# Kernel tuning notes

Hardware: AMD Instinct MI355X
Metric: run time of the kernel (lower is better)

## Reference

```python
import jax, jax.numpy as jnp
import numpy as np

ETA = 3.0
KCAP = 96
POS_W = 1.2
LAMBDA_CD = 1.0
LAMBDA_P0 = 1.0
STRIDES = (8.0, 16.0, 32.0)


def _level_terms(pred_reg, pred_obj, pred_cls, gt, stride):
    """Vectorized per-level version of the triple python loop.
    pred_reg: [B,6,H,W], pred_obj/pred_cls: [B,1,H,W], gt: [B,Ng,3,2].
    Returns partial sums (reg, obj, cls, pos_count, neg_count)."""
    B, _, H, W = pred_obj.shape
    HW = H * W
    Ng = gt.shape[1]
    ys = (jnp.arange(H, dtype=jnp.float32) + 0.5) * stride
    xs = (jnp.arange(W, dtype=jnp.float32) + 0.5) * stride
    yy, xx = jnp.meshgrid(ys, xs, indexing='ij')
    px = xx.reshape(-1)  # [HW]
    py = yy.reshape(-1)
    P = px[None, None, :]  # [1,1,HW]
    Q = py[None, None, :]
    # triangle vertices, each [B,Ng,1] for broadcasting against HW
    Ax, Ay = gt[:, :, 0, 0:1], gt[:, :, 0, 1:2]
    Bx, By = gt[:, :, 1, 0:1], gt[:, :, 1, 1:2]
    Cx, Cy = gt[:, :, 2, 0:1], gt[:, :, 2, 1:2]

    def sgn(x1, y1, x2, y2, x3, y3):
        return (x1 - x3) * (y2 - y3) - (x2 - x3) * (y1 - y3)

    d1 = sgn(P, Q, Ax, Ay, Bx, By)
    d2 = sgn(P, Q, Bx, By, Cx, Cy)
    d3 = sgn(P, Q, Cx, Cy, Ax, Ay)
    has_neg = (d1 < 0) | (d2 < 0) | (d3 < 0)
    has_pos = (d1 > 0) | (d2 > 0) | (d3 > 0)
    inside = ~(has_neg & has_pos)  # [B,Ng,HW]

    def segd(x1, y1, x2, y2):
        vx, vy = x2 - x1, y2 - y1
        wx, wy = P - x1, Q - y1
        t = jnp.clip((wx * vx + wy * vy) / (vx * vx + vy * vy + 1e-9), 0.0, 1.0)
        dx = P - (x1 + t * vx)
        dy = Q - (y1 + t * vy)
        return jnp.sqrt(dx * dx + dy * dy + 1e-12)

    dist = jnp.minimum(segd(Ax, Ay, Bx, By),
                       jnp.minimum(segd(Bx, By, Cx, Cy), segd(Cx, Cy, Ax, Ay)))
    pos = inside | (dist <= ETA)  # [B,Ng,HW]

    # top-k cap: keep the KCAP positives with smallest boundary distance
    dmask = jnp.where(pos, dist, jnp.inf)
    negd, idx = jax.lax.top_k(-dmask, KCAP)  # [B,Ng,K]
    keep = jnp.isfinite(negd)                # finite <=> was a positive
    bi = jnp.arange(B)[:, None, None]
    gi = jnp.arange(Ng)[None, :, None]
    capped = jnp.zeros((B, Ng, HW), dtype=bool).at[bi, gi, idx].set(keep)
    m = capped.astype(jnp.float32)
    pos_count = m.sum()

    # objectness BCE-with-logits (pos_weight) over the whole map
    obj_t = capped.any(axis=1).astype(jnp.float32)  # [B,HW]
    x = pred_obj.reshape(B, HW)
    obj_loss = (POS_W * obj_t * jax.nn.softplus(-x)
                + (1.0 - obj_t) * jax.nn.softplus(x)).sum()
    neg_count = jnp.float32(B * HW) - obj_t.sum()

    pred_off = pred_reg.transpose(0, 2, 3, 1).reshape(B, HW, 3, 2)
    centers = jnp.stack([px, py], axis=-1)  # [HW,2]
    gt_off = (gt[:, :, None] - centers[None, None, :, None]) / stride  # [B,Ng,HW,3,2]
    p0 = ((pred_off[:, None, :, 0] - gt_off[:, :, :, 0]) ** 2).sum(-1)  # [B,Ng,HW]
    pp = pred_off[:, None, :, 1:, :]  # [B,1,HW,2,2]
    gg = gt_off[:, :, :, 1:, :]       # [B,Ng,HW,2,2]
    d = jnp.sqrt(((pp[..., :, None, :] - gg[..., None, :, :]) ** 2).sum(-1))  # [B,Ng,HW,2,2]
    cd = d.min(-1).sum(-1) + d.min(-2).sum(-1)  # [B,Ng,HW]
    reg = (m * (LAMBDA_P0 * p0 + LAMBDA_CD * cd)).sum()

    # class BCE on positives only, target = 1
    cls = (m * jax.nn.softplus(-pred_cls.reshape(B, 1, HW))).sum()
    return reg, obj_loss, cls, pos_count, neg_count


def setup_inputs() -> dict:
    key = jax.random.key(0)
    ks = jax.random.split(key, 10)
    B, Ng = 16, 32
    shapes = [(128, 128), (64, 64), (32, 32)]
    inp = {}
    i = 0
    for l, (H, W) in enumerate(shapes):
        inp[f'pred_reg{l}'] = jax.random.normal(ks[i], (B, 6, H, W), dtype=jnp.float32); i += 1
        inp[f'pred_obj{l}'] = jax.random.normal(ks[i], (B, 1, H, W), dtype=jnp.float32); i += 1
        inp[f'pred_cls{l}'] = jax.random.normal(ks[i], (B, 1, H, W), dtype=jnp.float32); i += 1
    inp['gt'] = jax.random.uniform(ks[9], (B, Ng, 3, 2), dtype=jnp.float32) * 1024.0
    return inp


def reference(pred_reg0, pred_obj0, pred_cls0,
              pred_reg1, pred_obj1, pred_cls1,
              pred_reg2, pred_obj2, pred_cls2, gt):
    levels = [(pred_reg0, pred_obj0, pred_cls0),
              (pred_reg1, pred_obj1, pred_cls1),
              (pred_reg2, pred_obj2, pred_cls2)]
    reg = obj = cls = pc = nc = jnp.float32(0.0)
    for (pr, po, pcls), s in zip(levels, STRIDES):
        r, o, c, p, n = _level_terms(pr, po, pcls, gt, s)
        reg += r; obj += o; cls += c; pc += p; nc += n
    pos_eps = jnp.maximum(pc, 1.0)
    total = (reg / pos_eps
             + obj / (pos_eps + jnp.maximum(nc, 1.0))
             + cls / pos_eps)
    return total
```

## Files before the change

### kernel.cpp

```cpp
#include <hip/hip_runtime.h>

#define KCAP 96u
#define CAP 6144
#define PBLK 512
#define NTOT 344064
#define NPAIR 1536

__device__ __forceinline__ float softplus_f(float x) {
    return fmaxf(x, 0.0f) + log1pf(expf(-fabsf(x)));
}

__device__ __forceinline__ void tri_pos_dist(
    float px, float py,
    float ax, float ay, float bx, float by, float cx, float cy,
    bool& pos, float& dist)
{
#pragma clang fp contract(off)
    float d1 = (px - bx) * (ay - by) - (ax - bx) * (py - by);
    float d2 = (px - cx) * (by - cy) - (bx - cx) * (py - cy);
    float d3 = (px - ax) * (cy - ay) - (cx - ax) * (py - ay);
    bool has_neg = (d1 < 0.f) | (d2 < 0.f) | (d3 < 0.f);
    bool has_pos = (d1 > 0.f) | (d2 > 0.f) | (d3 > 0.f);
    bool inside = !(has_neg && has_pos);

    float dAB, dBC, dCA;
    {
        float vx = bx - ax, vy = by - ay, wx = px - ax, wy = py - ay;
        float t = (wx*vx + wy*vy) / (vx*vx + vy*vy + 1e-9f);
        t = fminf(fmaxf(t, 0.0f), 1.0f);
        float dx = px - (ax + t*vx), dy = py - (ay + t*vy);
        dAB = sqrtf(dx*dx + dy*dy + 1e-12f);
    }
    {
        float vx = cx - bx, vy = cy - by, wx = px - bx, wy = py - by;
        float t = (wx*vx + wy*vy) / (vx*vx + vy*vy + 1e-9f);
        t = fminf(fmaxf(t, 0.0f), 1.0f);
        float dx = px - (bx + t*vx), dy = py - (by + t*vy);
        dBC = sqrtf(dx*dx + dy*dy + 1e-12f);
    }
    {
        float vx = ax - cx, vy = ay - cy, wx = px - cx, wy = py - cy;
        float t = (wx*vx + wy*vy) / (vx*vx + vy*vy + 1e-9f);
        t = fminf(fmaxf(t, 0.0f), 1.0f);
        float dx = px - (cx + t*vx), dy = py - (cy + t*vy);
        dCA = sqrtf(dx*dx + dy*dy + 1e-12f);
    }
    dist = fminf(dAB, fminf(dBC, dCA));
    pos = inside || (dist <= 3.0f);
}

__global__ __launch_bounds__(PBLK) void select_kernel(
    const float* __restrict__ gt,
    unsigned* __restrict__ objbits,
    unsigned short* __restrict__ sel,
    unsigned* __restrict__ sel_cnt)
{
    const int bid = blockIdx.x;
    const int tid = threadIdx.x;
    const int lane = tid & 63;

    if (tid < 7) objbits[bid * 7 + tid] = 0u;

    const int level = bid >> 9;
    const int pair = bid & 511;

    int W, shift;
    float stride;
    if (level == 0)      { W = 128; shift = 7; stride = 8.0f;  }
    else if (level == 1) { W = 64;  shift = 6; stride = 16.0f; }
    else                 { W = 32;  shift = 5; stride = 32.0f; }

    const float* gp = gt + pair * 6;
    const float ax = gp[0], ay = gp[1];
    const float bx = gp[2], by = gp[3];
    const float cx = gp[4], cy = gp[5];

    const float inv = 1.0f / stride;
    float minx = fminf(ax, fminf(bx, cx)), maxx = fmaxf(ax, fmaxf(bx, cx));
    float miny = fminf(ay, fminf(by, cy)), maxy = fmaxf(ay, fmaxf(by, cy));
    int wlo = max(0,     (int)floorf((minx - 3.0f) * inv - 0.5f) - 1);
    int whi = min(W - 1, (int)ceilf ((maxx + 3.0f) * inv - 0.5f) + 1);
    int hlo = max(0,     (int)floorf((miny - 3.0f) * inv - 0.5f) - 1);
    int hhi = min(W - 1, (int)ceilf ((maxy + 3.0f) * inv - 0.5f) + 1);
    const int ncols = max(0, whi - wlo + 1);
    const int nb = (hhi - hlo + 1 > 0) ? (hhi - hlo + 1) * ncols : 0;
    const int nbR = (nb + PBLK - 1) & ~(PBLK - 1);
    const unsigned long long dmul =
        (ncols > 0) ? ((1ull << 40) / (unsigned)ncols + 1ull) : 0ull;

    __shared__ unsigned hist[2048];
    __shared__ unsigned chunk[256];
    __shared__ unsigned chunk4[64];
    __shared__ unsigned s_bits[CAP];
    __shared__ unsigned short s_hw[CAP];
    __shared__ unsigned s_cnt, s_T, s_k, s_tiecnt, s_sel;
    unsigned* tie_hw = hist;

    if (tid == 0) { s_cnt = 0u; s_tiecnt = 0u; s_sel = 0u; }
    for (int j = tid; j < 2048; j += PBLK) hist[j] = 0u;
    __syncthreads();

    auto kth_scan = [&](unsigned kk) {
        __syncthreads();
        if (tid < 256) {
            unsigned s = 0; int base = tid * 8;
            #pragma unroll
            for (int j = 0; j < 8; ++j) s += hist[base + j];
            chunk[tid] = s;
        }
        __syncthreads();
        if (tid < 64) {
            int b4 = tid * 4;
            chunk4[tid] = chunk[b4] + chunk[b4+1] + chunk[b4+2] + chunk[b4+3];
        }
        __syncthreads();
        if (tid == 0) {
            unsigned cum = 0; int t4 = 0;
            while (cum + chunk4[t4] < kk) { cum += chunk4[t4]; ++t4; }
            int t = t4 * 4;
            while (cum + chunk[t] < kk) { cum += chunk[t]; ++t; }
            int bb = t * 8;
            while (cum + hist[bb] < kk) { cum += hist[bb]; ++bb; }
            s_T = (unsigned)bb;
            s_k = kk - cum;
        }
        __syncthreads();
    };

    auto emit = [&](int hw) {
        unsigned slot = atomicAdd(&s_sel, 1u);
        sel[bid * 96 + slot] = (unsigned short)hw;
    };

    for (int i = tid; i < nbR; i += PBLK) {
        bool pos = false; unsigned bits = 0u; int hw = 0;
        if (i < nb) {
            int q = (int)(((unsigned long long)(unsigned)i * dmul) >> 40);
            int w = wlo + (i - q * ncols);
            int h = hlo + q;
            hw = (h << shift) | w;
            float px = (w + 0.5f) * stride;
            float py = (h + 0.5f) * stride;
            float dist;
            tri_pos_dist(px, py, ax, ay, bx, by, cx, cy, pos, dist);
            if (pos) { bits = __float_as_uint(dist); atomicAdd(&hist[bits >> 21], 1u); }
        }
        unsigned long long m = __ballot(pos);
        if (m) {
            int leader = __ffsll(m) - 1;
            unsigned base = 0u;
            if (lane == leader) base = atomicAdd(&s_cnt, (unsigned)__popcll(m));
            base = __shfl(base, leader);
            if (pos) {
                unsigned slot = base + (unsigned)__popcll(m & ((1ull << lane) - 1ull));
                if (slot < CAP) { s_bits[slot] = bits; s_hw[slot] = (unsigned short)hw; }
            }
        }
    }
    __syncthreads();

    const unsigned total = s_cnt;
    const bool fullsel = (total <= KCAP);
    unsigned n = min(total, (unsigned)CAP);
    unsigned kth_bits = 0u, tie_need = 0u;
    bool radix_fb = false;

    if (!fullsel) {
        kth_scan(KCAP);
        const unsigned T = s_T, kk1 = s_k;

        if (total > CAP) {
            if (tid == 0) s_cnt = 0u;
            __syncthreads();
            for (int i = tid; i < nbR; i += PBLK) {
                bool keep = false; unsigned bits = 0u; int hw = 0;
                if (i < nb) {
                    int q = (int)(((unsigned long long)(unsigned)i * dmul) >> 40);
                    int w = wlo + (i - q * ncols);
                    int h = hlo + q;
                    hw = (h << shift) | w;
                    float px = (w + 0.5f) * stride;
                    float py = (h + 0.5f) * stride;
                    bool pos; float dist;
                    tri_pos_dist(px, py, ax, ay, bx, by, cx, cy, pos, dist);
                    if (pos) {
                        bits = __float_as_uint(dist);
                        keep = ((bits >> 21) <= T);
                    }
                }
                unsigned long long m = __ballot(keep);
                if (m) {
                    int leader = __ffsll(m) - 1;
                    unsigned base = 0u;
                    if (lane == leader) base = atomicAdd(&s_cnt, (unsigned)__popcll(m));
                    base = __shfl(base, leader);
                    if (keep) {
                        unsigned slot = base + (unsigned)__popcll(m & ((1ull << lane) - 1ull));
                        if (slot < CAP) { s_bits[slot] = bits; s_hw[slot] = (unsigned short)hw; }
                    }
                }
            }
            __syncthreads();
            n = s_cnt;
            if (n > CAP) { radix_fb = true; }
        }

        if (!radix_fb) {
            __syncthreads();
            for (int j = tid; j < 2048; j += PBLK) hist[j] = 0u;
            __syncthreads();
            for (unsigned i = tid; i < n; i += PBLK) {
                unsigned bi = s_bits[i];
                if ((bi >> 21) == T) atomicAdd(&hist[(bi >> 10) & 0x7FFu], 1u);
            }
            kth_scan(kk1);
            unsigned prefix = (T << 11) | s_T;
            unsigned kk2 = s_k;
            __syncthreads();
            for (int j = tid; j < 2048; j += PBLK) hist[j] = 0u;
            __syncthreads();
            for (unsigned i = tid; i < n; i += PBLK) {
                unsigned bi = s_bits[i];
                if ((bi >> 10) == prefix) atomicAdd(&hist[bi & 0x3FFu], 1u);
            }
            kth_scan(kk2);
            kth_bits = (prefix << 10) | s_T;
            tie_need = s_k;
        }
    }

    if (fullsel) {
        for (unsigned i = tid; i < n; i += PBLK) emit((int)s_hw[i]);
    } else if (!radix_fb) {
        for (unsigned i = tid; i < n; i += PBLK) {
            unsigned bi = s_bits[i];
            if (bi < kth_bits) {
                emit((int)s_hw[i]);
            } else if (bi == kth_bits) {
                unsigned t = atomicAdd(&s_tiecnt, 1u);
                if (t < 2048u) tie_hw[t] = s_hw[i];
            }
        }
        __syncthreads();
        unsigned tn = min(s_tiecnt, 2048u);
        for (unsigned i = tid; i < tn; i += PBLK) {
            unsigned hwv = tie_hw[i], rank = 0;
            for (unsigned j = 0; j < tn; ++j) rank += (tie_hw[j] < hwv) ? 1u : 0u;
            if (rank < tie_need) emit((int)hwv);
        }
    } else {
        unsigned prefix = s_T;
        for (int p = 1; p < 3; ++p) {
            unsigned kk = s_k;
            __syncthreads();
            for (int j = tid; j < 2048; j += PBLK) hist[j] = 0u;
            __syncthreads();
            for (int i = tid; i < nb; i += PBLK) {
                int q = (int)(((unsigned long long)(unsigned)i * dmul) >> 40);
                int w = wlo + (i - q * ncols);
                int h = hlo + q;
                float px = (w + 0.5f) * stride;
                float py = (h + 0.5f) * stride;
                bool pos; float dist;
                tri_pos_dist(px, py, ax, ay, bx, by, cx, cy, pos, dist);
                if (!pos) continue;
                unsigned bits = __float_as_uint(dist);
                unsigned bin;
                if (p == 1) { if ((bits >> 21) != prefix) continue; bin = (bits >> 10) & 0x7FFu; }
                else        { if ((bits >> 10) != prefix) continue; bin = bits & 0x3FFu; }
                atomicAdd(&hist[bin], 1u);
            }
            kth_scan(kk);
            prefix = (p == 1) ? ((prefix << 11) | s_T) : ((prefix << 10) | s_T);
        }
        const unsigned kth = prefix, need = s_k;
        for (int i = tid; i < nb; i += PBLK) {
            int q = (int)(((unsigned long long)(unsigned)i * dmul) >> 40);
            int w = wlo + (i - q * ncols);
            int h = hlo + q;
            int hw = (h << shift) | w;
            float px = (w + 0.5f) * stride;
            float py = (h + 0.5f) * stride;
            bool pos; float dist;
            tri_pos_dist(px, py, ax, ay, bx, by, cx, cy, pos, dist);
            if (!pos) continue;
            unsigned bits = __float_as_uint(dist);
            if (bits < kth) {
                emit(hw);
            } else if (bits == kth) {
                unsigned t = atomicAdd(&s_tiecnt, 1u);
                if (t < 2048u) tie_hw[t] = (unsigned)hw;
            }
        }
        __syncthreads();
        unsigned tn = min(s_tiecnt, 2048u);
        for (unsigned i = tid; i < tn; i += PBLK) {
            unsigned hwv = tie_hw[i], rank = 0;
            for (unsigned j = 0; j < tn; ++j) rank += (tie_hw[j] < hwv) ? 1u : 0u;
            if (rank < need) emit((int)hwv);
        }
    }
    __syncthreads();
    if (tid == 0) sel_cnt[bid] = s_sel;
}

__global__ __launch_bounds__(256) void contrib_kernel(
    const float* __restrict__ gt,
    const float* __restrict__ reg0, const float* __restrict__ cls0, const float* __restrict__ o0,
    const float* __restrict__ reg1, const float* __restrict__ cls1, const float* __restrict__ o1,
    const float* __restrict__ reg2, const float* __restrict__ cls2, const float* __restrict__ o2,
    const unsigned short* __restrict__ sel, const unsigned* __restrict__ sel_cnt,
    unsigned* __restrict__ objbits,
    double* __restrict__ p_reg, double* __restrict__ p_cls,
    double* __restrict__ p_obj, unsigned* __restrict__ p_tc)
{
    const int bid = blockIdx.x;
    const int tid = threadIdx.x;

    double objAcc = 0.0;
    {
        int idx = bid * 256 + tid;
        if (idx < NTOT) {
            const float* o; int li;
            if (idx < 262144)      { o = o0; li = idx; }
            else if (idx < 327680) { o = o1; li = idx - 262144; }
            else                   { o = o2; li = idx - 327680; }
            objAcc = (double)softplus_f(o[li]);
        }
    }

    const int level = bid >> 9;
    const int pair = bid & 511;
    const int b = pair >> 5;
    int W, HW, shift, objbase;
    float stride;
    const float* pr; const float* pcl; const float* po;
    if (level == 0)      { W = 128; HW = 16384; shift = 7; stride = 8.0f;  objbase = 0;     pr = reg0; pcl = cls0; po = o0; }
    else if (level == 1) { W = 64;  HW = 4096;  shift = 6; stride = 16.0f; objbase = 8192;  pr = reg1; pcl = cls1; po = o1; }
    else                 { W = 32;  HW = 1024;  shift = 5; stride = 32.0f; objbase = 10240; pr = reg2; pcl = cls2; po = o2; }
    const int wmask = W - 1;
    const float inv = 1.0f / stride;

    const float* gp = gt + pair * 6;
    const float ax = gp[0], ay = gp[1];
    const float bx = gp[2], by = gp[3];
    const float cx = gp[4], cy = gp[5];

    const unsigned cnt = sel_cnt[bid];
    double regAcc = 0.0, clsAcc = 0.0;
    unsigned tcAcc = 0u;

    for (unsigned i = tid; i < cnt; i += 256) {
        int hw = (int)sel[bid * 96 + i];
        int h = hw >> shift, w = hw & wmask;
        float px = (w + 0.5f) * stride;
        float py = (h + 0.5f) * stride;
        const float* base = pr + (size_t)b * 6 * HW + hw;
        float p0x = base[0],          p0y = base[HW];
        float p1x = base[2 * HW],     p1y = base[3 * HW];
        float p2x = base[4 * HW],     p2y = base[5 * HW];
        float g0x = (ax - px) * inv,  g0y = (ay - py) * inv;
        float g1x = (bx - px) * inv,  g1y = (by - py) * inv;
        float g2x = (cx - px) * inv,  g2y = (cy - py) * inv;
        float dx0 = p0x - g0x, dy0 = p0y - g0y;
        float p0t = dx0 * dx0 + dy0 * dy0;
        float e11x = p1x - g1x, e11y = p1y - g1y;
        float e12x = p1x - g2x, e12y = p1y - g2y;
        float e21x = p2x - g1x, e21y = p2y - g1y;
        float e22x = p2x - g2x, e22y = p2y - g2y;
        float d11 = sqrtf(e11x * e11x + e11y * e11y);
        float d12 = sqrtf(e12x * e12x + e12y * e12y);
        float d21 = sqrtf(e21x * e21x + e21y * e21y);
        float d22 = sqrtf(e22x * e22x + e22y * e22y);
        float cd = fminf(d11, d12) + fminf(d21, d22) + fminf(d11, d21) + fminf(d12, d22);
        regAcc += (double)(p0t + cd);
        clsAcc += (double)softplus_f(-pcl[(size_t)b * HW + hw]);

        unsigned bi = (unsigned)(b * HW + hw);
        unsigned bit = 1u << (bi & 31u);
        unsigned old = atomicOr(&objbits[objbase + (bi >> 5)], bit);
        if (!(old & bit)) {
            float x = po[(size_t)b * HW + hw];
            float spx = softplus_f(x);
            objAcc += (double)(1.2f * softplus_f(-x)) - (double)spx;
            tcAcc += 1u;
        }
    }

    for (int off = 32; off > 0; off >>= 1) {
        regAcc += __shfl_down(regAcc, off);
        clsAcc += __shfl_down(clsAcc, off);
        objAcc += __shfl_down(objAcc, off);
        tcAcc  += __shfl_down(tcAcc, off);
    }
    __shared__ double rr[4], rc[4], ro[4];
    __shared__ unsigned rt[4];
    int wave = tid >> 6, lane = tid & 63;
    if (lane == 0) { rr[wave] = regAcc; rc[wave] = clsAcc; ro[wave] = objAcc; rt[wave] = tcAcc; }
    __syncthreads();
    if (tid == 0) {
        p_reg[bid] = rr[0] + rr[1] + rr[2] + rr[3];
        p_cls[bid] = rc[0] + rc[1] + rc[2] + rc[3];
        p_obj[bid] = ro[0] + ro[1] + ro[2] + ro[3];
        p_tc[bid]  = rt[0] + rt[1] + rt[2] + rt[3];
    }
}

__global__ __launch_bounds__(1024) void finalize_kernel(
    const double* __restrict__ p_reg, const double* __restrict__ p_cls,
    const double* __restrict__ p_obj, const unsigned* __restrict__ p_tc,
    const unsigned* __restrict__ sel_cnt,
    float* __restrict__ out)
{
    const int tid = threadIdx.x;
    double reg = 0.0, cls = 0.0, obj = 0.0;
    unsigned pc = 0u, tc = 0u;
    for (int i = tid; i < NPAIR; i += 1024) {
        reg += p_reg[i]; cls += p_cls[i]; obj += p_obj[i];
        tc += p_tc[i]; pc += sel_cnt[i];
    }
    for (int off = 32; off > 0; off >>= 1) {
        reg += __shfl_down(reg, off);
        cls += __shfl_down(cls, off);
        obj += __shfl_down(obj, off);
        pc  += __shfl_down(pc, off);
        tc  += __shfl_down(tc, off);
    }
    __shared__ double rr[16], rc[16], ro[16];
    __shared__ unsigned rp[16], rn[16];
    int wave = tid >> 6, lane = tid & 63;
    if (lane == 0) { rr[wave] = reg; rc[wave] = cls; ro[wave] = obj; rp[wave] = pc; rn[wave] = tc; }
    __syncthreads();
    if (tid == 0) {
        double sreg = 0, scls = 0, sobj = 0; unsigned spc = 0, stc = 0;
        #pragma unroll
        for (int i = 0; i < 16; ++i) {
            sreg += rr[i]; scls += rc[i]; sobj += ro[i]; spc += rp[i]; stc += rn[i];
        }
        double nc = (double)NTOT - (double)stc;
        double pos_eps = fmax((double)spc, 1.0);
        double den = pos_eps + fmax(nc, 1.0);
        out[0] = (float)(sreg / pos_eps + sobj / den + scls / pos_eps);
    }
}

extern "C" void kernel_launch(void* const* d_in, const int* in_sizes, int n_in,
                              void* d_out, int out_size, void* d_ws, size_t ws_size,
                              hipStream_t stream)
{
    (void)in_sizes; (void)n_in; (void)out_size; (void)ws_size;
    const float* reg0 = (const float*)d_in[0];
    const float* obj0 = (const float*)d_in[1];
    const float* cls0 = (const float*)d_in[2];
    const float* reg1 = (const float*)d_in[3];
    const float* obj1 = (const float*)d_in[4];
    const float* cls1 = (const float*)d_in[5];
    const float* reg2 = (const float*)d_in[6];
    const float* obj2 = (const float*)d_in[7];
    const float* cls2 = (const float*)d_in[8];
    const float* gt   = (const float*)d_in[9];

    char* ws = (char*)d_ws;
    unsigned*       objbits = (unsigned*)ws;
    unsigned short* sel     = (unsigned short*)(ws + 43008);
    unsigned*       sel_cnt = (unsigned*)(ws + 337920);
    double*         p_reg   = (double*)(ws + 344064);
    double*         p_cls   = (double*)(ws + 356352);
    double*         p_obj   = (double*)(ws + 368640);
    unsigned*       p_tc    = (unsigned*)(ws + 380928);

    select_kernel<<<NPAIR, PBLK, 0, stream>>>(gt, objbits, sel, sel_cnt);
    contrib_kernel<<<NPAIR, 256, 0, stream>>>(gt,
                                              reg0, cls0, obj0,
                                              reg1, cls1, obj1,
                                              reg2, cls2, obj2,
                                              sel, sel_cnt, objbits,
                                              p_reg, p_cls, p_obj, p_tc);
    finalize_kernel<<<1, 1024, 0, stream>>>(p_reg, p_cls, p_obj, p_tc, sel_cnt,
                                            (float*)d_out);
}
```

Before: 139.4 us.

## Fuse selection and contribution kernels into one per-pair kernel

Merges the top-k selection kernel and the loss-contribution kernel into a single pair kernel that computes each selected cell's contribution right away, instead of writing selected indices to global memory and reading them back. The objbits bitmap is now cleared by a separate small zero kernel so that the atomicOr dedup still works across blocks. The objectness softplus sweep over the full map is spread over 224 cells per block inside the fused kernel. The change removes the sel round trip and one kernel boundary, but adds a launch, and the fused kernel carries more registers and shared memory, which may lower occupancy.

```diff
diff --git a/kernel.cpp b/kernel.cpp
--- a/kernel.cpp
+++ b/kernel.cpp
@@ -5,6 +5,7 @@
 #define PBLK 512
 #define NTOT 344064
 #define NPAIR 1536
+#define CELLS_PB 224
 
 __device__ __forceinline__ float softplus_f(float x) {
     return fmaxf(x, 0.0f) + log1pf(expf(-fabsf(x)));
@@ -49,26 +50,46 @@
     pos = inside || (dist <= 3.0f);
 }
 
-__global__ __launch_bounds__(PBLK) void select_kernel(
+__global__ void zero_kernel(unsigned* __restrict__ p, int n) {
+    int i = blockIdx.x * 256 + threadIdx.x;
+    if (i < n) p[i] = 0u;
+}
+
+__global__ __launch_bounds__(PBLK) void pair_kernel(
     const float* __restrict__ gt,
+    const float* __restrict__ reg0, const float* __restrict__ cls0, const float* __restrict__ o0,
+    const float* __restrict__ reg1, const float* __restrict__ cls1, const float* __restrict__ o1,
+    const float* __restrict__ reg2, const float* __restrict__ cls2, const float* __restrict__ o2,
     unsigned* __restrict__ objbits,
-    unsigned short* __restrict__ sel,
-    unsigned* __restrict__ sel_cnt)
+    double* __restrict__ p_reg, double* __restrict__ p_cls,
+    double* __restrict__ p_obj, unsigned* __restrict__ p_tc,
+    unsigned* __restrict__ p_pos)
 {
     const int bid = blockIdx.x;
     const int tid = threadIdx.x;
     const int lane = tid & 63;
 
-    if (tid < 7) objbits[bid * 7 + tid] = 0u;
-
     const int level = bid >> 9;
     const int pair = bid & 511;
-
-    int W, shift;
+    const int b = pair >> 5;
+
+    int W, HW, shift, objbase;
     float stride;
-    if (level == 0)      { W = 128; shift = 7; stride = 8.0f;  }
-    else if (level == 1) { W = 64;  shift = 6; stride = 16.0f; }
-    else                 { W = 32;  shift = 5; stride = 32.0f; }
+    const float* pr; const float* pcl; const float* po;
+    if (level == 0)      { W = 128; HW = 16384; shift = 7; stride = 8.0f;  objbase = 0;     pr = reg0; pcl = cls0; po = o0; }
+    else if (level == 1) { W = 64;  HW = 4096;  shift = 6; stride = 16.0f; objbase = 8192;  pr = reg1; pcl = cls1; po = o1; }
+    else                 { W = 32;  HW = 1024;  shift = 5; stride = 32.0f; objbase = 10240; pr = reg2; pcl = cls2; po = o2; }
+    const int wmask = W - 1;
+
+    double objAcc = 0.0;
+    if (tid < CELLS_PB) {
+        int idx = bid * CELLS_PB + tid;
+        const float* o; int li;
+        if (idx < 262144)      { o = o0; li = idx; }
+        else if (idx < 327680) { o = o1; li = idx - 262144; }
+        else                   { o = o2; li = idx - 327680; }
+        objAcc = (double)softplus_f(o[li]);
+    }
 
     const float* gp = gt + pair * 6;
     const float ax = gp[0], ay = gp[1];
@@ -93,10 +114,12 @@
     __shared__ unsigned chunk4[64];
     __shared__ unsigned s_bits[CAP];
     __shared__ unsigned short s_hw[CAP];
-    __shared__ unsigned s_cnt, s_T, s_k, s_tiecnt, s_sel;
+    __shared__ unsigned s_cnt, s_T, s_k, s_tiecnt;
+    __shared__ double red_reg[8], red_cls[8], red_obj[8];
+    __shared__ unsigned red_tc[8], red_pos[8];
     unsigned* tie_hw = hist;
 
-    if (tid == 0) { s_cnt = 0u; s_tiecnt = 0u; s_sel = 0u; }
+    if (tid == 0) { s_cnt = 0u; s_tiecnt = 0u; }
     for (int j = tid; j < 2048; j += PBLK) hist[j] = 0u;
     __syncthreads();
 
@@ -125,11 +148,6 @@
             s_k = kk - cum;
         }
         __syncthreads();
-    };
-
-    auto emit = [&](int hw) {
-        unsigned slot = atomicAdd(&s_sel, 1u);
-        sel[bid * 96 + slot] = (unsigned short)hw;
     };
 
     for (int i = tid; i < nbR; i += PBLK) {
@@ -229,129 +247,10 @@
         }
     }
 
-    if (fullsel) {
-        for (unsigned i = tid; i < n; i += PBLK) emit((int)s_hw[i]);
-    } else if (!radix_fb) {
-        for (unsigned i = tid; i < n; i += PBLK) {
-            unsigned bi = s_bits[i];
-            if (bi < kth_bits) {
-                emit((int)s_hw[i]);
-            } else if (bi == kth_bits) {
-                unsigned t = atomicAdd(&s_tiecnt, 1u);
-                if (t < 2048u) tie_hw[t] = s_hw[i];
-            }
-        }
-        __syncthreads();
-        unsigned tn = min(s_tiecnt, 2048u);
-        for (unsigned i = tid; i < tn; i += PBLK) {
-            unsigned hwv = tie_hw[i], rank = 0;
-            for (unsigned j = 0; j < tn; ++j) rank += (tie_hw[j] < hwv) ? 1u : 0u;
-            if (rank < tie_need) emit((int)hwv);
-        }
-    } else {
-        unsigned prefix = s_T;
-        for (int p = 1; p < 3; ++p) {
-            unsigned kk = s_k;
-            __syncthreads();
-            for (int j = tid; j < 2048; j += PBLK) hist[j] = 0u;
-            __syncthreads();
-            for (int i = tid; i < nb; i += PBLK) {
-                int q = (int)(((unsigned long long)(unsigned)i * dmul) >> 40);
-                int w = wlo + (i - q * ncols);
-                int h = hlo + q;
-                float px = (w + 0.5f) * stride;
-                float py = (h + 0.5f) * stride;
-                bool pos; float dist;
-                tri_pos_dist(px, py, ax, ay, bx, by, cx, cy, pos, dist);
-                if (!pos) continue;
-                unsigned bits = __float_as_uint(dist);
-                unsigned bin;
-                if (p == 1) { if ((bits >> 21) != prefix) continue; bin = (bits >> 10) & 0x7FFu; }
-                else        { if ((bits >> 10) != prefix) continue; bin = bits & 0x3FFu; }
-                atomicAdd(&hist[bin], 1u);
-            }
-            kth_scan(kk);
-            prefix = (p == 1) ? ((prefix << 11) | s_T) : ((prefix << 10) | s_T);
-        }
-        const unsigned kth = prefix, need = s_k;
-        for (int i = tid; i < nb; i += PBLK) {
-            int q = (int)(((unsigned long long)(unsigned)i * dmul) >> 40);
-            int w = wlo + (i - q * ncols);
-            int h = hlo + q;
-            int hw = (h << shift) | w;
-            float px = (w + 0.5f) * stride;
-            float py = (h + 0.5f) * stride;
-            bool pos; float dist;
-            tri_pos_dist(px, py, ax, ay, bx, by, cx, cy, pos, dist);
-            if (!pos) continue;
-            unsigned bits = __float_as_uint(dist);
-            if (bits < kth) {
-                emit(hw);
-            } else if (bits == kth) {
-                unsigned t = atomicAdd(&s_tiecnt, 1u);
-                if (t < 2048u) tie_hw[t] = (unsigned)hw;
-            }
-        }
-        __syncthreads();
-        unsigned tn = min(s_tiecnt, 2048u);
-        for (unsigned i = tid; i < tn; i += PBLK) {
-            unsigned hwv = tie_hw[i], rank = 0;
-            for (unsigned j = 0; j < tn; ++j) rank += (tie_hw[j] < hwv) ? 1u : 0u;
-            if (rank < need) emit((int)hwv);
-        }
-    }
-    __syncthreads();
-    if (tid == 0) sel_cnt[bid] = s_sel;
-}
-
-__global__ __launch_bounds__(256) void contrib_kernel(
-    const float* __restrict__ gt,
-    const float* __restrict__ reg0, const float* __restrict__ cls0, const float* __restrict__ o0,
-    const float* __restrict__ reg1, const float* __restrict__ cls1, const float* __restrict__ o1,
-    const float* __restrict__ reg2, const float* __restrict__ cls2, const float* __restrict__ o2,
-    const unsigned short* __restrict__ sel, const unsigned* __restrict__ sel_cnt,
-    unsigned* __restrict__ objbits,
-    double* __restrict__ p_reg, double* __restrict__ p_cls,
-    double* __restrict__ p_obj, unsigned* __restrict__ p_tc)
-{
-    const int bid = blockIdx.x;
-    const int tid = threadIdx.x;
-
-    double objAcc = 0.0;
-    {
-        int idx = bid * 256 + tid;
-        if (idx < NTOT) {
-            const float* o; int li;
-            if (idx < 262144)      { o = o0; li = idx; }
-            else if (idx < 327680) { o = o1; li = idx - 262144; }
-            else                   { o = o2; li = idx - 327680; }
-            objAcc = (double)softplus_f(o[li]);
-        }
-    }
-
-    const int level = bid >> 9;
-    const int pair = bid & 511;
-    const int b = pair >> 5;
-    int W, HW, shift, objbase;
-    float stride;
-    const float* pr; const float* pcl; const float* po;
-    if (level == 0)      { W = 128; HW = 16384; shift = 7; stride = 8.0f;  objbase = 0;     pr = reg0; pcl = cls0; po = o0; }
-    else if (level == 1) { W = 64;  HW = 4096;  shift = 6; stride = 16.0f; objbase = 8192;  pr = reg1; pcl = cls1; po = o1; }
-    else                 { W = 32;  HW = 1024;  shift = 5; stride = 32.0f; objbase = 10240; pr = reg2; pcl = cls2; po = o2; }
-    const int wmask = W - 1;
-    const float inv = 1.0f / stride;
-
-    const float* gp = gt + pair * 6;
-    const float ax = gp[0], ay = gp[1];
-    const float bx = gp[2], by = gp[3];
-    const float cx = gp[4], cy = gp[5];
-
-    const unsigned cnt = sel_cnt[bid];
     double regAcc = 0.0, clsAcc = 0.0;
-    unsigned tcAcc = 0u;
-
-    for (unsigned i = tid; i < cnt; i += 256) {
-        int hw = (int)sel[bid * 96 + i];
+    unsigned tcAcc = 0u, posAcc = 0u;
+
+    auto contribute = [&](int hw) {
         int h = hw >> shift, w = hw & wmask;
         float px = (w + 0.5f) * stride;
         float py = (h + 0.5f) * stride;
@@ -375,15 +274,87 @@
         float cd = fminf(d11, d12) + fminf(d21, d22) + fminf(d11, d21) + fminf(d12, d22);
         regAcc += (double)(p0t + cd);
         clsAcc += (double)softplus_f(-pcl[(size_t)b * HW + hw]);
+        posAcc += 1u;
 
         unsigned bi = (unsigned)(b * HW + hw);
         unsigned bit = 1u << (bi & 31u);
         unsigned old = atomicOr(&objbits[objbase + (bi >> 5)], bit);
         if (!(old & bit)) {
             float x = po[(size_t)b * HW + hw];
-            float spx = softplus_f(x);
-            objAcc += (double)(1.2f * softplus_f(-x)) - (double)spx;
+            objAcc += (double)(1.2f * softplus_f(-x)) - (double)softplus_f(x);
             tcAcc += 1u;
+        }
+    };
+
+    if (fullsel) {
+        for (unsigned i = tid; i < n; i += PBLK) contribute((int)s_hw[i]);
+    } else if (!radix_fb) {
+        for (unsigned i = tid; i < n; i += PBLK) {
+            unsigned bi = s_bits[i];
+            if (bi < kth_bits) {
+                contribute((int)s_hw[i]);
+            } else if (bi == kth_bits) {
+                unsigned t = atomicAdd(&s_tiecnt, 1u);
+                if (t < 2048u) tie_hw[t] = s_hw[i];
+            }
+        }
+        __syncthreads();
+        unsigned tn = min(s_tiecnt, 2048u);
+        for (unsigned i = tid; i < tn; i += PBLK) {
+            unsigned hwv = tie_hw[i], rank = 0;
+            for (unsigned j = 0; j < tn; ++j) rank += (tie_hw[j] < hwv) ? 1u : 0u;
+            if (rank < tie_need) contribute((int)hwv);
+        }
+    } else {
+        unsigned prefix = s_T;
+        for (int p = 1; p < 3; ++p) {
+            unsigned kk = s_k;
+            __syncthreads();
+            for (int j = tid; j < 2048; j += PBLK) hist[j] = 0u;
+            __syncthreads();
+            for (int i = tid; i < nb; i += PBLK) {
+                int q = (int)(((unsigned long long)(unsigned)i * dmul) >> 40);
+                int w = wlo + (i - q * ncols);
+                int h = hlo + q;
+                float px = (w + 0.5f) * stride;
+                float py = (h + 0.5f) * stride;
+                bool pos; float dist;
+                tri_pos_dist(px, py, ax, ay, bx, by, cx, cy, pos, dist);
+                if (!pos) continue;
+                unsigned bits = __float_as_uint(dist);
+                unsigned bin;
+                if (p == 1) { if ((bits >> 21) != prefix) continue; bin = (bits >> 10) & 0x7FFu; }
+                else        { if ((bits >> 10) != prefix) continue; bin = bits & 0x3FFu; }
+                atomicAdd(&hist[bin], 1u);
+            }
+            kth_scan(kk);
+            prefix = (p == 1) ? ((prefix << 11) | s_T) : ((prefix << 10) | s_T);
+        }
+        const unsigned kth = prefix, need = s_k;
+        for (int i = tid; i < nb; i += PBLK) {
+            int q = (int)(((unsigned long long)(unsigned)i * dmul) >> 40);
+            int w = wlo + (i - q * ncols);
+            int h = hlo + q;
+            int hw = (h << shift) | w;
+            float px = (w + 0.5f) * stride;
+            float py = (h + 0.5f) * stride;
+            bool pos; float dist;
+            tri_pos_dist(px, py, ax, ay, bx, by, cx, cy, pos, dist);
+            if (!pos) continue;
+            unsigned bits = __float_as_uint(dist);
+            if (bits < kth) {
+                contribute(hw);
+            } else if (bits == kth) {
+                unsigned t = atomicAdd(&s_tiecnt, 1u);
+                if (t < 2048u) tie_hw[t] = (unsigned)hw;
+            }
+        }
+        __syncthreads();
+        unsigned tn = min(s_tiecnt, 2048u);
+        for (unsigned i = tid; i < tn; i += PBLK) {
+            unsigned hwv = tie_hw[i], rank = 0;
+            for (unsigned j = 0; j < tn; ++j) rank += (tie_hw[j] < hwv) ? 1u : 0u;
+            if (rank < need) contribute((int)hwv);
         }
     }
 
@@ -392,24 +363,33 @@
         clsAcc += __shfl_down(clsAcc, off);
         objAcc += __shfl_down(objAcc, off);
         tcAcc  += __shfl_down(tcAcc, off);
-    }
-    __shared__ double rr[4], rc[4], ro[4];
-    __shared__ unsigned rt[4];
-    int wave = tid >> 6, lane = tid & 63;
-    if (lane == 0) { rr[wave] = regAcc; rc[wave] = clsAcc; ro[wave] = objAcc; rt[wave] = tcAcc; }
+        posAcc += __shfl_down(posAcc, off);
+    }
+    int wave = tid >> 6;
+    if (lane == 0) {
+        red_reg[wave] = regAcc; red_cls[wave] = clsAcc; red_obj[wave] = objAcc;
+        red_tc[wave] = tcAcc; red_pos[wave] = posAcc;
+    }
     __syncthreads();
     if (tid == 0) {
-        p_reg[bid] = rr[0] + rr[1] + rr[2] + rr[3];
-        p_cls[bid] = rc[0] + rc[1] + rc[2] + rc[3];
-        p_obj[bid] = ro[0] + ro[1] + ro[2] + ro[3];
-        p_tc[bid]  = rt[0] + rt[1] + rt[2] + rt[3];
+        double rs = 0.0, cs = 0.0, os = 0.0; unsigned ts = 0u, ps = 0u;
+        #pragma unroll
+        for (int i = 0; i < 8; ++i) {
+            rs += red_reg[i]; cs += red_cls[i]; os += red_obj[i];
+            ts += red_tc[i]; ps += red_pos[i];
+        }
+        p_reg[bid] = rs;
+        p_cls[bid] = cs;
+        p_obj[bid] = os;
+        p_tc[bid]  = ts;
+        p_pos[bid] = ps;
     }
 }
 
 __global__ __launch_bounds__(1024) void finalize_kernel(
     const double* __restrict__ p_reg, const double* __restrict__ p_cls,
     const double* __restrict__ p_obj, const unsigned* __restrict__ p_tc,
-    const unsigned* __restrict__ sel_cnt,
+    const unsigned* __restrict__ p_pos,
     float* __restrict__ out)
 {
     const int tid = threadIdx.x;
@@ -417,7 +397,7 @@
     unsigned pc = 0u, tc = 0u;
     for (int i = tid; i < NPAIR; i += 1024) {
         reg += p_reg[i]; cls += p_cls[i]; obj += p_obj[i];
-        tc += p_tc[i]; pc += sel_cnt[i];
+        tc += p_tc[i]; pc += p_pos[i];
     }
     for (int off = 32; off > 0; off >>= 1) {
         reg += __shfl_down(reg, off);
@@ -461,21 +441,20 @@
     const float* gt   = (const float*)d_in[9];
 
     char* ws = (char*)d_ws;
-    unsigned*       objbits = (unsigned*)ws;
-    unsigned short* sel     = (unsigned short*)(ws + 43008);
-    unsigned*       sel_cnt = (unsigned*)(ws + 337920);
-    double*         p_reg   = (double*)(ws + 344064);
-    double*         p_cls   = (double*)(ws + 356352);
-    double*         p_obj   = (double*)(ws + 368640);
-    unsigned*       p_tc    = (unsigned*)(ws + 380928);
-
-    select_kernel<<<NPAIR, PBLK, 0, stream>>>(gt, objbits, sel, sel_cnt);
-    contrib_kernel<<<NPAIR, 256, 0, stream>>>(gt,
-                                              reg0, cls0, obj0,
-                                              reg1, cls1, obj1,
-                                              reg2, cls2, obj2,
-                                              sel, sel_cnt, objbits,
-                                              p_reg, p_cls, p_obj, p_tc);
-    finalize_kernel<<<1, 1024, 0, stream>>>(p_reg, p_cls, p_obj, p_tc, sel_cnt,
+    unsigned* objbits = (unsigned*)ws;
+    double*   p_reg   = (double*)(ws + 43008);
+    double*   p_cls   = (double*)(ws + 55296);
+    double*   p_obj   = (double*)(ws + 67584);
+    unsigned* p_tc    = (unsigned*)(ws + 79872);
+    unsigned* p_pos   = (unsigned*)(ws + 86016);
+
+    zero_kernel<<<42, 256, 0, stream>>>(objbits, 10752);
+    pair_kernel<<<NPAIR, PBLK, 0, stream>>>(gt,
+                                            reg0, cls0, obj0,
+                                            reg1, cls1, obj1,
+                                            reg2, cls2, obj2,
+                                            objbits,
+                                            p_reg, p_cls, p_obj, p_tc, p_pos);
+    finalize_kernel<<<1, 1024, 0, stream>>>(p_reg, p_cls, p_obj, p_tc, p_pos,
                                             (float*)d_out);
 }
```

Measured after the change: 145.1 us. 1.04x slower.
